# Kernel optimization log

Measured on AMD Instinct MI355X. Metric: run time of the kernel, lower is better.

Reference implementation:

```python
import jax, jax.numpy as jnp
import numpy as np
import math

HIDDEN = 1024
HEADS = 16
HEAD_DIM = HIDDEN // HEADS


def setup_inputs() -> dict:
    key = jax.random.key(0)
    ks = jax.random.split(key, 9)
    s = 1.0 / math.sqrt(HIDDEN)
    return {
        "x": jax.random.normal(ks[0], (4, 2048, HIDDEN), dtype=jnp.float32),
        "Wq": jax.random.normal(ks[1], (HIDDEN, HIDDEN), dtype=jnp.float32) * s,
        "bq": jnp.zeros((HIDDEN,), dtype=jnp.float32),
        "Wk": jax.random.normal(ks[2], (HIDDEN, HIDDEN), dtype=jnp.float32) * s,
        "bk": jnp.zeros((HIDDEN,), dtype=jnp.float32),
        "Wv": jax.random.normal(ks[3], (HIDDEN, HIDDEN), dtype=jnp.float32) * s,
        "bv": jnp.zeros((HIDDEN,), dtype=jnp.float32),
        "Wo": jax.random.normal(ks[4], (HIDDEN, HIDDEN), dtype=jnp.float32) * s,
        "bo": jnp.zeros((HIDDEN,), dtype=jnp.float32),
    }


def reference(x, Wq, bq, Wk, bk, Wv, bv, Wo, bo):
    B, L, D = x.shape
    H, hd = HEADS, HEAD_DIM
    # QKV projections (weights stored as [in, out], i.e. torch W.T)
    q = (x @ Wq + bq).reshape(B, L, H, hd).transpose(0, 2, 1, 3)  # [B,H,L,hd]
    k = (x @ Wk + bk).reshape(B, L, H, hd).transpose(0, 2, 1, 3)
    v = (x @ Wv + bv).reshape(B, L, H, hd).transpose(0, 2, 1, 3)
    scores = jnp.einsum("bhqd,bhkd->bhqk", q, k) / math.sqrt(hd)  # [B,H,L,L]
    causal_mask = jnp.triu(jnp.full((L, L), -jnp.inf, dtype=scores.dtype), k=1)
    att = jax.nn.softmax(scores + causal_mask, axis=-1)
    out = jnp.einsum("bhqk,bhkd->bhqd", att, v)  # [B,H,L,hd]
    out = out.transpose(0, 2, 1, 3).reshape(B, L, D)
    return out @ Wo + bo
```

## Files before the change

kernel.cpp:

```cpp
#include <hip/hip_runtime.h>
#include <stdint.h>

#define LOG2E 1.44269504088896340736f

typedef __attribute__((ext_vector_type(8))) short short8;
typedef __attribute__((ext_vector_type(4))) float float4v;

typedef const __attribute__((address_space(1))) unsigned int gu32;
typedef __attribute__((address_space(3))) unsigned int lu32;

__device__ __forceinline__ void async16(const unsigned short* g, unsigned short* l){
  __builtin_amdgcn_global_load_lds((gu32*)g, (lu32*)l, 16, 0, 0);
}

__device__ __forceinline__ unsigned short f2bf(float f){
  union { float f; unsigned int u; } v; v.f = f;
  unsigned int u = v.u;
  return (unsigned short)((u + 0x7FFFu + ((u >> 16) & 1u)) >> 16);
}
__device__ __forceinline__ unsigned int pkbf(float a, float b){
  union { float f; unsigned int u; } ua, ub; ua.f=a; ub.f=b;
  return ((ua.u + 0x8000u) >> 16) | ((ub.u + 0x8000u) & 0xFFFF0000u);
}

__global__ void convert_x_kernel(const float* __restrict__ x, unsigned short* __restrict__ xb){
  int t = blockIdx.x * 256 + threadIdx.x;
  const float4v* xp = (const float4v*)x;
  float4v a = xp[2*t], b = xp[2*t+1];
  short8 o;
  o[0]=(short)f2bf(a[0]); o[1]=(short)f2bf(a[1]); o[2]=(short)f2bf(a[2]); o[3]=(short)f2bf(a[3]);
  o[4]=(short)f2bf(b[0]); o[5]=(short)f2bf(b[1]); o[6]=(short)f2bf(b[2]); o[7]=(short)f2bf(b[3]);
  ((short8*)xb)[t] = o;
}

__global__ void transpose_w_kernel(const float* __restrict__ Wq, const float* __restrict__ Wk,
                                   const float* __restrict__ Wv, const float* __restrict__ Wo,
                                   unsigned short* __restrict__ wqkvT, unsigned short* __restrict__ woT){
  __shared__ float tileS[64][68];
  int mat = blockIdx.x >> 8, tile = blockIdx.x & 255;
  int tk = tile >> 4, tn = tile & 15;
  const float* W = (mat==0)?Wq:(mat==1)?Wk:(mat==2)?Wv:Wo;
  int k0 = tk*64, n0 = tn*64;
  int tid = threadIdx.x;
  #pragma unroll
  for (int it=0; it<4; ++it){
    int idx = tid + it*256;
    int r = idx >> 4, c4 = idx & 15;
    float4v v = *(const float4v*)&W[(uint64_t)(k0+r)*1024 + n0 + c4*4];
    tileS[r][c4*4+0]=v[0]; tileS[r][c4*4+1]=v[1]; tileS[r][c4*4+2]=v[2]; tileS[r][c4*4+3]=v[3];
  }
  __syncthreads();
  unsigned short* dst; int nbase;
  if (mat<3){ dst = wqkvT; nbase = mat*1024 + n0; } else { dst = woT; nbase = n0; }
  #pragma unroll
  for (int it=0; it<2; ++it){
    int idx = tid + it*256;
    int n = idx >> 3, g = idx & 7;
    short8 o;
    #pragma unroll
    for (int j=0;j<8;++j) o[j] = (short)f2bf(tileS[g*8+j][n]);
    *(short8*)&dst[(uint64_t)(nbase+n)*1024 + k0 + g*8] = o;
  }
}

template<int EPI>
__global__ __launch_bounds__(256, 2) void gemm_kernel(
    const unsigned short* __restrict__ A, const unsigned short* __restrict__ BT,
    const float* __restrict__ bias0, const float* __restrict__ bias1, const float* __restrict__ bias2,
    unsigned short* __restrict__ oq, unsigned short* __restrict__ ok,
    unsigned short* __restrict__ ov, float* __restrict__ of)
{
  __shared__ __attribute__((aligned(16))) unsigned short lS[2*128*64];
  unsigned short* lA = lS;
  unsigned short* lB = lS + 128*64;
  const int tid = threadIdx.x, lane = tid & 63, wave = tid >> 6;
  const int wr = wave >> 1, wc = wave & 1;
  const int by = blockIdx.x & 63, bx = blockIdx.x >> 6;
  const int m0 = by * 128, n0 = bx * 128;
  const int c = lane & 15, quad = lane >> 4;
  const float QSCALE = 0.125f * LOG2E;

  float4v acc[4][4];
  #pragma unroll
  for (int i=0;i<4;++i)
    #pragma unroll
    for (int j=0;j<4;++j) acc[i][j] = (float4v){0.f,0.f,0.f,0.f};

  for (int kt = 0; kt < 16; ++kt){
    __syncthreads();
    #pragma unroll
    for (int it=0; it<4; ++it){
      int gl = (wave*4+it)*64 + lane;
      int row = gl >> 3, gp = gl & 7, gs = gp ^ (row & 7);
      async16(&A[(uint64_t)(m0+row)*1024 + kt*64 + gs*8], &lA[gl*8]);
    }
    #pragma unroll
    for (int it=0; it<4; ++it){
      int gl = (wave*4+it)*64 + lane;
      int row = gl >> 3, gp = gl & 7, gs = gp ^ (row & 7);
      async16(&BT[(uint64_t)(n0+row)*1024 + kt*64 + gs*8], &lB[gl*8]);
    }
    __syncthreads();
    #pragma unroll
    for (int kk=0; kk<2; ++kk){
      short8 af[4], bf[4];
      #pragma unroll
      for (int i=0;i<4;++i){
        int row = wr*64 + i*16 + c;
        int g = (quad + kk*4) ^ (row & 7);
        af[i] = *(const short8*)&lA[row*64 + g*8];
      }
      #pragma unroll
      for (int j=0;j<4;++j){
        int row = wc*64 + j*16 + c;
        int g = (quad + kk*4) ^ (row & 7);
        bf[j] = *(const short8*)&lB[row*64 + g*8];
      }
      #pragma unroll
      for (int i=0;i<4;++i)
        #pragma unroll
        for (int j=0;j<4;++j)
          acc[i][j] = __builtin_amdgcn_mfma_f32_16x16x32_bf16(af[i], bf[j], acc[i][j], 0, 0, 0);
    }
  }

  if (EPI == 0){
    const int sel = bx >> 3;
    const int n0l = n0 & 1023;
    const int h0 = n0l >> 6;
    const int bb = m0 >> 11, l0 = m0 & 2047;
    const float* bp = (sel==0)?bias0:(sel==1)?bias1:bias2;
    float bj[4];
    #pragma unroll
    for (int j=0;j<4;++j) bj[j] = bp[n0l + wc*64 + j*16 + c];
    __syncthreads();
    if (sel < 2){
      unsigned short* dst = (sel==0)?oq:ok;
      #pragma unroll
      for (int i=0;i<4;++i){
        #pragma unroll
        for (int r=0;r<4;++r){
          int mloc = wr*64 + i*16 + quad*4 + r;
          #pragma unroll
          for (int j=0;j<4;++j){
            float v = acc[i][j][r] + bj[j];
            if (sel == 0) v *= QSCALE;
            int col = wc*64 + j*16 + c;
            int gg = col >> 3;
            int gs2 = (gg & 8) | ((gg & 7) ^ (mloc & 7));
            lS[mloc*128 + gs2*8 + (col & 7)] = f2bf(v);
          }
        }
      }
      __syncthreads();
      #pragma unroll
      for (int it=0; it<8; ++it){
        int gl = it*256 + tid;
        int row = gl >> 4, gg = gl & 15;
        int gs2 = (gg & 8) | ((gg & 7) ^ (row & 7));
        short8 w = *(const short8*)&lS[row*128 + gs2*8];
        int hh = h0 + (gg >> 3);
        *(short8*)&dst[((uint64_t)(bb*16 + hh)*2048 + l0 + row)*64 + (gg & 7)*8] = w;
      }
    } else {
      #pragma unroll
      for (int i=0;i<4;++i){
        #pragma unroll
        for (int r=0;r<4;++r){
          int mloc = wr*64 + i*16 + quad*4 + r;
          int mgg = mloc >> 3;
          #pragma unroll
          for (int j=0;j<4;++j){
            float v = acc[i][j][r] + bj[j];
            int col = wc*64 + j*16 + c;
            int gsT = (mgg & 8) | ((mgg & 7) ^ (col & 7));
            lS[col*128 + gsT*8 + (mloc & 7)] = f2bf(v);
          }
        }
      }
      __syncthreads();
      #pragma unroll
      for (int it=0; it<8; ++it){
        int idx = it*256 + tid;
        int mg = idx & 15, cc = idx >> 4;
        int gsT2 = (mg & 8) | ((mg & 7) ^ (cc & 7));
        short8 w = *(const short8*)&lS[cc*128 + gsT2*8];
        int hh = h0 + (cc >> 6), d = cc & 63;
        *(short8*)&ov[((uint64_t)(bb*16 + hh)*64 + d)*2048 + l0 + mg*8] = w;
      }
    }
  } else {
    float* lf = (float*)lS;
    float bj[4];
    #pragma unroll
    for (int j=0;j<4;++j) bj[j] = bias0[n0 + wc*64 + j*16 + c];
    #pragma unroll
    for (int half=0; half<2; ++half){
      __syncthreads();
      if (wr == half){
        #pragma unroll
        for (int i=0;i<4;++i){
          #pragma unroll
          for (int r=0;r<4;++r){
            int lrow = i*16 + quad*4 + r;
            #pragma unroll
            for (int j=0;j<4;++j){
              int col = wc*64 + j*16 + c;
              int gg = col >> 2;
              int gs2 = (gg & 24) | ((gg & 7) ^ (lrow & 7));
              lf[lrow*128 + gs2*4 + (col & 3)] = acc[i][j][r] + bj[j];
            }
          }
        }
      }
      __syncthreads();
      #pragma unroll
      for (int it=0; it<8; ++it){
        int gl = it*256 + tid;
        int lrow = gl >> 5, gg = gl & 31;
        int gs2 = (gg & 24) | ((gg & 7) ^ (lrow & 7));
        float4v w = *(const float4v*)&lf[lrow*128 + gs2*4];
        *(float4v*)&of[(uint64_t)(m0 + half*64 + lrow)*1024 + n0 + gg*4] = w;
      }
    }
  }
}

__global__ __launch_bounds__(256, 2) void attn_kernel(
    const unsigned short* __restrict__ q, const unsigned short* __restrict__ k,
    const unsigned short* __restrict__ vt, unsigned short* __restrict__ o)
{
  __shared__ __attribute__((aligned(16))) unsigned short lQ[128*64];
  __shared__ __attribute__((aligned(16))) unsigned short lK[2][64*64];
  __shared__ __attribute__((aligned(16))) unsigned short lV[2][64*64];
  __shared__ __attribute__((aligned(16))) unsigned short lP[4][32*64];

  const int idx = blockIdx.x;
  const int bh = idx & 63;
  const int qt = 15 - (idx >> 6);
  const int tid = threadIdx.x, lane = tid & 63, wave = tid >> 6;
  const int c = lane & 15, quad = lane >> 4;

  const unsigned short* qh = q  + (uint64_t)bh * (2048*64);
  const unsigned short* kh = k  + (uint64_t)bh * (2048*64);
  const unsigned short* vh = vt + (uint64_t)bh * (64*2048);

  #pragma unroll
  for (int it=0; it<4; ++it){
    int gl = (wave*4+it)*64 + lane;
    int row = gl >> 3, gp = gl & 7, gs = gp ^ (row & 7);
    async16(&qh[(uint64_t)(qt*128 + row)*64 + gs*8], &lQ[gl*8]);
  }
  #pragma unroll
  for (int it=0; it<2; ++it){
    int gl = (wave*2+it)*64 + lane;
    int row = gl >> 3, gp = gl & 7, gs = gp ^ (row & 7);
    async16(&kh[(uint64_t)row*64 + gs*8], &lK[0][gl*8]);
    async16(&vh[(uint64_t)row*2048 + gs*8], &lV[0][gl*8]);
  }

  float4v accO[2][4];
  #pragma unroll
  for (int u=0;u<2;++u)
    #pragma unroll
    for (int t=0;t<4;++t) accO[u][t] = (float4v){0.f,0.f,0.f,0.f};
  float lsum[2] = {0.f, 0.f};
  short8 qf[2][2];

  const int ktEnd = 2*qt + 1;
  unsigned short* Pw = &lP[wave][0];

  for (int kt = 0; kt <= ktEnd; ++kt){
    __syncthreads();
    const int cb = kt & 1;

    if (kt == 0){
      #pragma unroll
      for (int u=0; u<2; ++u)
        #pragma unroll
        for (int kk=0; kk<2; ++kk){
          int row = u*64 + wave*16 + c;
          int g = (kk*4 + quad) ^ (row & 7);
          qf[u][kk] = *(const short8*)&lQ[row*64 + g*8];
        }
    }
    if (kt < ktEnd){
      const int nb = 1 - cb;
      #pragma unroll
      for (int it=0; it<2; ++it){
        int gl = (wave*2+it)*64 + lane;
        int row = gl >> 3, gp = gl & 7, gs = gp ^ (row & 7);
        async16(&kh[(uint64_t)((kt+1)*64 + row)*64 + gs*8], &lK[nb][gl*8]);
        async16(&vh[(uint64_t)row*2048 + (kt+1)*64 + gs*8], &lV[nb][gl*8]);
      }
    }

    const bool doU0 = (kt != ktEnd);

    float4v s[2][4];
    #pragma unroll
    for (int u=0;u<2;++u)
      #pragma unroll
      for (int j=0;j<4;++j) s[u][j] = (float4v){0.f,0.f,0.f,0.f};
    #pragma unroll
    for (int kk=0; kk<2; ++kk){
      short8 kf[4];
      #pragma unroll
      for (int j=0;j<4;++j){
        int row = j*16 + c;
        int g = (kk*4 + quad) ^ (row & 7);
        kf[j] = *(const short8*)&lK[cb][row*64 + g*8];
      }
      #pragma unroll
      for (int j=0;j<4;++j)
        s[1][j] = __builtin_amdgcn_mfma_f32_16x16x32_bf16(kf[j], qf[1][kk], s[1][j], 0, 0, 0);
      if (doU0){
        #pragma unroll
        for (int j=0;j<4;++j)
          s[0][j] = __builtin_amdgcn_mfma_f32_16x16x32_bf16(kf[j], qf[0][kk], s[0][j], 0, 0, 0);
      }
    }

    #pragma unroll
    for (int u=0;u<2;++u){
      if (u==0 && !doU0) continue;
      const int qb_u = qt*128 + u*64 + wave*16;
      const bool needMask = (kt*64 + 63 > qb_u);
      const int qg = qb_u + c;
      #pragma unroll
      for (int j=0;j<4;++j){
        float p0,p1,p2,p3;
        {
          float4v sv = s[u][j];
          p0 = __builtin_amdgcn_exp2f(sv[0]);
          p1 = __builtin_amdgcn_exp2f(sv[1]);
          p2 = __builtin_amdgcn_exp2f(sv[2]);
          p3 = __builtin_amdgcn_exp2f(sv[3]);
        }
        if (needMask){
          int keyb = kt*64 + j*16 + quad*4;
          if (keyb + 0 > qg) p0 = 0.f;
          if (keyb + 1 > qg) p1 = 0.f;
          if (keyb + 2 > qg) p2 = 0.f;
          if (keyb + 3 > qg) p3 = 0.f;
        }
        lsum[u] += (p0 + p1) + (p2 + p3);
        int row = u*16 + c;
        int g = (2*j + (quad>>1)) ^ (row & 7);
        uint2 w; w.x = pkbf(p0,p1); w.y = pkbf(p2,p3);
        *(uint2*)&Pw[row*64 + g*8 + (quad&1)*4] = w;
      }
    }

    #pragma unroll
    for (int kk=0; kk<2; ++kk){
      short8 bv[4];
      #pragma unroll
      for (int t=0;t<4;++t){
        int row = t*16 + c;
        int g = (kk*4 + quad) ^ (row & 7);
        bv[t] = *(const short8*)&lV[cb][row*64 + g*8];
      }
      {
        int row = 16 + c;
        int g = (kk*4 + quad) ^ (row & 7);
        short8 ap = *(const short8*)&Pw[row*64 + g*8];
        #pragma unroll
        for (int t=0;t<4;++t)
          accO[1][t] = __builtin_amdgcn_mfma_f32_16x16x32_bf16(ap, bv[t], accO[1][t], 0, 0, 0);
      }
      if (doU0){
        int row = c;
        int g = (kk*4 + quad) ^ (row & 7);
        short8 ap = *(const short8*)&Pw[row*64 + g*8];
        #pragma unroll
        for (int t=0;t<4;++t)
          accO[0][t] = __builtin_amdgcn_mfma_f32_16x16x32_bf16(ap, bv[t], accO[0][t], 0, 0, 0);
      }
    }
  }

  #pragma unroll
  for (int u=0;u<2;++u){
    lsum[u] += __shfl_xor(lsum[u], 16, 64);
    lsum[u] += __shfl_xor(lsum[u], 32, 64);
  }

  const int b = bh >> 4, h = bh & 15;
  unsigned short* lPf = &lP[0][0];
  #pragma unroll
  for (int u=0;u<2;++u){
    #pragma unroll
    for (int r=0;r<4;++r){
      float ls = __shfl(lsum[u], quad*4 + r, 64);
      float rinv = 1.0f / ls;
      int mloc = u*64 + wave*16 + quad*4 + r;
      #pragma unroll
      for (int t=0;t<4;++t){
        int col = t*16 + c;
        int gg = col >> 3;
        int gs2 = gg ^ (mloc & 7);
        lPf[mloc*64 + gs2*8 + (col & 7)] = f2bf(accO[u][t][r] * rinv);
      }
    }
  }
  __syncthreads();
  #pragma unroll
  for (int it=0; it<4; ++it){
    int gl = it*256 + tid;
    int row = gl >> 3, gg = gl & 7;
    int gs2 = gg ^ (row & 7);
    short8 w = *(const short8*)&lPf[row*64 + gs2*8];
    uint64_t m = (uint64_t)b*2048 + qt*128 + row;
    *(short8*)&o[m*1024 + h*64 + gg*8] = w;
  }
}

extern "C" void kernel_launch(void* const* d_in, const int* in_sizes, int n_in,
                              void* d_out, int out_size, void* d_ws, size_t ws_size,
                              hipStream_t stream)
{
  (void)in_sizes; (void)n_in; (void)out_size; (void)ws_size;
  const float* x  = (const float*)d_in[0];
  const float* Wq = (const float*)d_in[1];
  const float* bq = (const float*)d_in[2];
  const float* Wk = (const float*)d_in[3];
  const float* bk = (const float*)d_in[4];
  const float* Wv = (const float*)d_in[5];
  const float* bv = (const float*)d_in[6];
  const float* Wo = (const float*)d_in[7];
  const float* bo = (const float*)d_in[8];
  float* out = (float*)d_out;

  char* ws = (char*)d_ws;
  unsigned short* xb    = (unsigned short*)(ws);
  unsigned short* wqkvT = (unsigned short*)(ws + (16ull<<20));
  unsigned short* woT   = (unsigned short*)(ws + (22ull<<20));
  unsigned short* qb    = (unsigned short*)(ws + (24ull<<20));
  unsigned short* kb    = (unsigned short*)(ws + (40ull<<20));
  unsigned short* vtb   = (unsigned short*)(ws + (56ull<<20));
  unsigned short* ab    = xb;

  convert_x_kernel<<<4096, 256, 0, stream>>>(x, xb);
  transpose_w_kernel<<<1024, 256, 0, stream>>>(Wq, Wk, Wv, Wo, wqkvT, woT);
  gemm_kernel<0><<<1536, 256, 0, stream>>>(xb, wqkvT, bq, bk, bv, qb, kb, vtb, nullptr);
  attn_kernel<<<1024, 256, 0, stream>>>(qb, kb, vtb, ab);
  gemm_kernel<1><<<512, 256, 0, stream>>>(ab, woT, bo, nullptr, nullptr, nullptr, nullptr, nullptr, out);
}
```

Measured before the change: 247.0 us.

## Keep Q and P fragments in registers via permlane swaps, raise attention occupancy

The attention kernel no longer stages Q or the softmax probabilities P in LDS. Q fragments are loaded straight from global memory into registers, and P is rearranged into the MFMA A-operand layout with permlane32/permlane16 swap instructions. This cuts LDS from 64KB to 32KB, so launch bounds go from 2 to 4 blocks per CU, and the output staging now reuses the K buffer behind an added barrier. The query-tile dispatch order is also changed to interleave heavy and light causal tiles. The risk is higher register pressure at the new occupancy target, and the permlane layout must exactly match the previous LDS layout to stay correct.

Result: slower. 264.1 us (+6.9%).

```diff
diff --git a/kernel.cpp b/kernel.cpp
--- a/kernel.cpp
+++ b/kernel.cpp
@@ -5,6 +5,8 @@
 
 typedef __attribute__((ext_vector_type(8))) short short8;
 typedef __attribute__((ext_vector_type(4))) float float4v;
+typedef __attribute__((ext_vector_type(4))) unsigned int uint4v;
+typedef __attribute__((ext_vector_type(2))) unsigned int uint2v;
 
 typedef const __attribute__((address_space(1))) unsigned int gu32;
 typedef __attribute__((address_space(3))) unsigned int lu32;
@@ -21,6 +23,23 @@
 __device__ __forceinline__ unsigned int pkbf(float a, float b){
   union { float f; unsigned int u; } ua, ub; ua.f=a; ub.f=b;
   return ((ua.u + 0x8000u) >> 16) | ((ub.u + 0x8000u) & 0xFFFF0000u);
+}
+
+__device__ __forceinline__ void pl32(unsigned int &a, unsigned int &b){
+#if __has_builtin(__builtin_amdgcn_permlane32_swap)
+  uint2v r = __builtin_amdgcn_permlane32_swap(a, b, false, false);
+  a = r[0]; b = r[1];
+#else
+  asm("v_permlane32_swap_b32 %0, %1" : "+v"(a), "+v"(b));
+#endif
+}
+__device__ __forceinline__ void pl16(unsigned int &a, unsigned int &b){
+#if __has_builtin(__builtin_amdgcn_permlane16_swap)
+  uint2v r = __builtin_amdgcn_permlane16_swap(a, b, false, false);
+  a = r[0]; b = r[1];
+#else
+  asm("v_permlane16_swap_b32 %0, %1" : "+v"(a), "+v"(b));
+#endif
 }
 
 __global__ void convert_x_kernel(const float* __restrict__ x, unsigned short* __restrict__ xb){
@@ -226,18 +245,18 @@
   }
 }
 
-__global__ __launch_bounds__(256, 2) void attn_kernel(
+__global__ __launch_bounds__(256, 4) void attn_kernel(
     const unsigned short* __restrict__ q, const unsigned short* __restrict__ k,
     const unsigned short* __restrict__ vt, unsigned short* __restrict__ o)
 {
-  __shared__ __attribute__((aligned(16))) unsigned short lQ[128*64];
   __shared__ __attribute__((aligned(16))) unsigned short lK[2][64*64];
   __shared__ __attribute__((aligned(16))) unsigned short lV[2][64*64];
-  __shared__ __attribute__((aligned(16))) unsigned short lP[4][32*64];
 
   const int idx = blockIdx.x;
   const int bh = idx & 63;
-  const int qt = 15 - (idx >> 6);
+  const int g4 = idx >> 8;
+  const int u4 = (idx >> 6) & 3;
+  const int qt = (g4==0) ? (15 - u4) : (g4==1) ? (8 + u4) : (g4==2) ? (7 - u4) : u4;
   const int tid = threadIdx.x, lane = tid & 63, wave = tid >> 6;
   const int c = lane & 15, quad = lane >> 4;
 
@@ -245,12 +264,15 @@
   const unsigned short* kh = k  + (uint64_t)bh * (2048*64);
   const unsigned short* vh = vt + (uint64_t)bh * (64*2048);
 
-  #pragma unroll
-  for (int it=0; it<4; ++it){
-    int gl = (wave*4+it)*64 + lane;
-    int row = gl >> 3, gp = gl & 7, gs = gp ^ (row & 7);
-    async16(&qh[(uint64_t)(qt*128 + row)*64 + gs*8], &lQ[gl*8]);
-  }
+  short8 qf[2][2];
+  #pragma unroll
+  for (int u=0;u<2;++u)
+    #pragma unroll
+    for (int kk=0;kk<2;++kk){
+      int row = qt*128 + u*64 + wave*16 + c;
+      qf[u][kk] = *(const short8*)&qh[(uint64_t)row*64 + (kk*4+quad)*8];
+    }
+
   #pragma unroll
   for (int it=0; it<2; ++it){
     int gl = (wave*2+it)*64 + lane;
@@ -265,25 +287,13 @@
     #pragma unroll
     for (int t=0;t<4;++t) accO[u][t] = (float4v){0.f,0.f,0.f,0.f};
   float lsum[2] = {0.f, 0.f};
-  short8 qf[2][2];
 
   const int ktEnd = 2*qt + 1;
-  unsigned short* Pw = &lP[wave][0];
 
   for (int kt = 0; kt <= ktEnd; ++kt){
     __syncthreads();
     const int cb = kt & 1;
 
-    if (kt == 0){
-      #pragma unroll
-      for (int u=0; u<2; ++u)
-        #pragma unroll
-        for (int kk=0; kk<2; ++kk){
-          int row = u*64 + wave*16 + c;
-          int g = (kk*4 + quad) ^ (row & 7);
-          qf[u][kk] = *(const short8*)&lQ[row*64 + g*8];
-        }
-    }
     if (kt < ktEnd){
       const int nb = 1 - cb;
       #pragma unroll
@@ -321,12 +331,14 @@
       }
     }
 
-    #pragma unroll
-    for (int u=0;u<2;++u){
+    short8 pa[2][2];
+    #pragma unroll
+    for (int u=1;u>=0;--u){
       if (u==0 && !doU0) continue;
       const int qb_u = qt*128 + u*64 + wave*16;
       const bool needMask = (kt*64 + 63 > qb_u);
       const int qg = qb_u + c;
+      unsigned int w[4][2];
       #pragma unroll
       for (int j=0;j<4;++j){
         float p0,p1,p2,p3;
@@ -345,10 +357,17 @@
           if (keyb + 3 > qg) p3 = 0.f;
         }
         lsum[u] += (p0 + p1) + (p2 + p3);
-        int row = u*16 + c;
-        int g = (2*j + (quad>>1)) ^ (row & 7);
-        uint2 w; w.x = pkbf(p0,p1); w.y = pkbf(p2,p3);
-        *(uint2*)&Pw[row*64 + g*8 + (quad&1)*4] = w;
+        w[j][0] = pkbf(p0,p1);
+        w[j][1] = pkbf(p2,p3);
+      }
+      #pragma unroll
+      for (int kk=0;kk<2;++kk){
+        unsigned int a0 = w[2*kk+0][0], b0 = w[2*kk+1][0];
+        unsigned int a1 = w[2*kk+0][1], b1 = w[2*kk+1][1];
+        pl32(a0,b0); pl32(a1,b1);
+        pl16(a0,b0); pl16(a1,b1);
+        uint4v uv; uv[0]=a0; uv[1]=a1; uv[2]=b0; uv[3]=b1;
+        pa[u][kk] = __builtin_bit_cast(short8, uv);
       }
     }
 
@@ -361,21 +380,13 @@
         int g = (kk*4 + quad) ^ (row & 7);
         bv[t] = *(const short8*)&lV[cb][row*64 + g*8];
       }
-      {
-        int row = 16 + c;
-        int g = (kk*4 + quad) ^ (row & 7);
-        short8 ap = *(const short8*)&Pw[row*64 + g*8];
+      #pragma unroll
+      for (int t=0;t<4;++t)
+        accO[1][t] = __builtin_amdgcn_mfma_f32_16x16x32_bf16(pa[1][kk], bv[t], accO[1][t], 0, 0, 0);
+      if (doU0){
         #pragma unroll
         for (int t=0;t<4;++t)
-          accO[1][t] = __builtin_amdgcn_mfma_f32_16x16x32_bf16(ap, bv[t], accO[1][t], 0, 0, 0);
-      }
-      if (doU0){
-        int row = c;
-        int g = (kk*4 + quad) ^ (row & 7);
-        short8 ap = *(const short8*)&Pw[row*64 + g*8];
-        #pragma unroll
-        for (int t=0;t<4;++t)
-          accO[0][t] = __builtin_amdgcn_mfma_f32_16x16x32_bf16(ap, bv[t], accO[0][t], 0, 0, 0);
+          accO[0][t] = __builtin_amdgcn_mfma_f32_16x16x32_bf16(pa[0][kk], bv[t], accO[0][t], 0, 0, 0);
       }
     }
   }
@@ -386,8 +397,10 @@
     lsum[u] += __shfl_xor(lsum[u], 32, 64);
   }
 
+  __syncthreads();
+
   const int b = bh >> 4, h = bh & 15;
-  unsigned short* lPf = &lP[0][0];
+  unsigned short* lPf = &lK[0][0];
   #pragma unroll
   for (int u=0;u<2;++u){
     #pragma unroll
```
